# Optimization experiments

Hardware: AMD Instinct MI355X
Metric: run time of the kernel (lower is better)

Reference implementation:

```python
import jax, jax.numpy as jnp
import numpy as np

N_NODES = 10000
N_EDGES = 160000
NUM_FEAT = 14
EDGE_DIM = 4
DIM = 64        # hidden_channels
HID = 128       # GENConv MLP expansion = 2
LAYERS = 28
MSG_EPS = 1e-7  # GENConv eps added to relu(message)
LN_EPS = 1e-5   # torch LayerNorm default


def layernorm(h, g, b):
    mu = jnp.mean(h, axis=-1, keepdims=True)
    var = jnp.mean(jnp.square(h - mu), axis=-1, keepdims=True)
    return (h - mu) * jax.lax.rsqrt(var + LN_EPS) * g + b


def gen_conv(x, ea, src, dst, t, W1, b1, g1, be1, W2, b2):
    # message: relu(x_j + edge_attr) + eps  -> [E, D]
    msg = jax.nn.relu(x[src] + ea) + MSG_EPS
    # softmax aggregation over edges grouped by destination node
    logits = msg * t
    m = jax.ops.segment_max(logits, dst, num_segments=N_NODES)
    e = jnp.exp(logits - m[dst])
    s = jax.ops.segment_sum(e, dst, num_segments=N_NODES)
    alpha = e / (s[dst] + 1e-16)
    agg = jax.ops.segment_sum(msg * alpha, dst, num_segments=N_NODES)
    # residual + MLP [D -> 2D -> D] with LayerNorm+ReLU in between
    h = agg + x
    h = jax.nn.relu(layernorm(h @ W1 + b1, g1, be1))
    return h @ W2 + b2


def setup_inputs() -> dict:
    key = jax.random.key(0)
    ks = jax.random.split(key, 24)
    sc = 0.05
    inp = {
        "x": jax.random.normal(ks[0], (N_NODES, NUM_FEAT), jnp.float32),
        "edge_attr": jax.random.normal(ks[1], (N_EDGES, EDGE_DIM), jnp.float32),
        "src": jax.random.randint(ks[2], (N_EDGES,), 0, N_NODES, jnp.int32),
        "dst": jax.random.randint(ks[3], (N_EDGES,), 0, N_NODES, jnp.int32),
        # encoders
        "W_node": jax.random.normal(ks[4], (NUM_FEAT, DIM), jnp.float32) * sc,
        "b_node": jnp.zeros((DIM,), jnp.float32),
        "W_edge": jax.random.normal(ks[5], (EDGE_DIM, DIM), jnp.float32) * sc,
        "b_edge": jnp.zeros((DIM,), jnp.float32),
        # per-layer GENConv params (stacked over LAYERS)
        "t": jnp.ones((LAYERS,), jnp.float32),
        "W1": jax.random.normal(ks[6], (LAYERS, DIM, HID), jnp.float32) * sc,
        "b1": jnp.zeros((LAYERS, HID), jnp.float32),
        "g1": jnp.ones((LAYERS, HID), jnp.float32),
        "be1": jnp.zeros((LAYERS, HID), jnp.float32),
        "W2": jax.random.normal(ks[7], (LAYERS, HID, DIM), jnp.float32) * sc,
        "b2": jnp.zeros((LAYERS, DIM), jnp.float32),
        # per-layer DeepGCNLayer LayerNorm
        "ln_g": jnp.ones((LAYERS, DIM), jnp.float32),
        "ln_b": jnp.zeros((LAYERS, DIM), jnp.float32),
        # output projection
        "W_out": jax.random.normal(ks[8], (DIM, DIM), jnp.float32) * sc,
        "b_out": jnp.zeros((DIM,), jnp.float32),
    }
    return inp


def reference(x, edge_attr, src, dst, W_node, b_node, W_edge, b_edge,
              t, W1, b1, g1, be1, W2, b2, ln_g, ln_b, W_out, b_out):
    h = x @ W_node + b_node                  # node encoder  [N, D]
    ea = edge_attr @ W_edge + b_edge         # edge encoder  [E, D]

    # layer 0: conv only (no res+ wrapper), per DeeperGCN.forward
    h = gen_conv(h, ea, src, dst, t[0], W1[0], b1[0], g1[0], be1[0], W2[0], b2[0])

    # layers 1..L-1: res+ block: x + conv(dropout(relu(norm(x))))  (eval: dropout = id)
    def step(hc, p):
        ti, w1, bb1, gg1, bbe1, w2, bb2, lg, lb = p
        u = jax.nn.relu(layernorm(hc, lg, lb))
        u = gen_conv(u, ea, src, dst, ti, w1, bb1, gg1, bbe1, w2, bb2)
        return hc + u, None

    rest = (t[1:], W1[1:], b1[1:], g1[1:], be1[1:], W2[1:], b2[1:], ln_g[1:], ln_b[1:])
    h, _ = jax.lax.scan(step, h, rest)

    # final: act(layers[0].norm(x)), dropout (eval: id), lin
    h = jax.nn.relu(layernorm(h, ln_g[0], ln_b[0]))
    return h @ W_out + b_out
```

## Files before the change

### kernel.cpp

```cpp
#include <hip/hip_runtime.h>
#include <hip/hip_cooperative_groups.h>

namespace cg = cooperative_groups;

#define N_NODES 10000
#define N_EDGES 160000
#define NUM_FEAT 14
#define DIM 64
#define HID 128
#define LAYERS 28

#define NPB 20
#define NLB (N_NODES / NPB)
#define TPB 640

__device__ __forceinline__ void stage16(const float* gsrc, float* lds_base) {
  __builtin_amdgcn_global_load_lds(
      (const __attribute__((address_space(1))) void*)gsrc,
      (__attribute__((address_space(3))) void*)lds_base, 16, 0, 0);
}


__global__ __launch_bounds__(256) void k_hist(const int* __restrict__ dst, int* __restrict__ cur) {
  int e = blockIdx.x * 256 + threadIdx.x;
  if (e < N_EDGES) atomicAdd(&cur[dst[e]], 1);
}

__global__ __launch_bounds__(256) void k_scan(int* __restrict__ cur, int* __restrict__ off) {
  __shared__ int part[256];
  int t = threadIdx.x;
  const int CH = 40;
  int base = t * CH;
  int s = 0;
  for (int i = 0; i < CH; i++) {
    int idx = base + i;
    if (idx < N_NODES) s += cur[idx];
  }
  part[t] = s;
  __syncthreads();
  for (int ofs = 1; ofs < 256; ofs <<= 1) {
    int tmp = (t >= ofs) ? part[t - ofs] : 0;
    __syncthreads();
    part[t] += tmp;
    __syncthreads();
  }
  int run = part[t] - s;
  for (int i = 0; i < CH; i++) {
    int idx = base + i;
    if (idx < N_NODES) {
      int d = cur[idx];
      off[idx] = run;
      cur[idx] = run;
      run += d;
    }
  }
  if (t == 255) off[N_NODES] = part[255];
}

__global__ __launch_bounds__(256) void k_scatter(const int* __restrict__ dst, int* __restrict__ cur,
                                                 int* __restrict__ eids) {
  int e = blockIdx.x * 256 + threadIdx.x;
  if (e < N_EDGES) {
    int p = atomicAdd(&cur[dst[e]], 1);
    eids[p] = e;
  }
}

__global__ __launch_bounds__(256) void k_sortgather(
    const int* __restrict__ off, const int* __restrict__ eids,
    const int* __restrict__ src, const float4* __restrict__ eattr,
    const float* __restrict__ W_edge, const float* __restrict__ b_edge,
    int* __restrict__ src_s, float4* __restrict__ eattr_s, float* __restrict__ ea_s) {
  int node = blockIdx.x * 4 + (threadIdx.x >> 6);
  int lane = threadIdx.x & 63;
  if (node >= N_NODES) return;
  float we0 = W_edge[lane], we1 = W_edge[64 + lane], we2 = W_edge[128 + lane],
        we3 = W_edge[192 + lane];
  float be = b_edge[lane];
  int a = off[node];
  int d = off[node + 1] - a;
  if (d <= 64) {
    int key = (lane < d) ? eids[a + lane] : 0x7fffffff;
#pragma unroll
    for (int k = 2; k <= 64; k <<= 1) {
      for (int j = k >> 1; j > 0; j >>= 1) {
        int p = __shfl_xor(key, j);
        bool dirUp = ((lane & k) == 0);
        bool isLower = ((lane & j) == 0);
        key = ((isLower == dirUp) ? min(key, p) : max(key, p));
      }
    }
    float4 ev = make_float4(0.f, 0.f, 0.f, 0.f);
    if (lane < d) {
      src_s[a + lane] = src[key];
      ev = eattr[key];
    }
    for (int j = 0; j < d; j++) {
      float ex = __shfl(ev.x, j), ey = __shfl(ev.y, j),
            ez = __shfl(ev.z, j), ew = __shfl(ev.w, j);
      ea_s[(size_t)(a + j) * 64 + lane] =
          be + ex * we0 + ey * we1 + ez * we2 + ew * we3;
    }
  } else {
    for (int i = lane; i < d; i += 64) {
      int e = eids[a + i];
      int r = 0;
      for (int j = 0; j < d; j++) r += (eids[a + j] < e) ? 1 : 0;
      src_s[a + r] = src[e];
      eattr_s[a + r] = eattr[e];
    }
    for (int j = 0; j < d; j++) {
      float4 e4 = eattr_s[a + j];
      ea_s[(size_t)(a + j) * 64 + lane] =
          be + e4.x * we0 + e4.y * we1 + e4.z * we2 + e4.w * we3;
    }
  }
}


__global__ __launch_bounds__(256) void k_enc(const float* __restrict__ x, const float* __restrict__ Wn,
                                             const float* __restrict__ bn, float* __restrict__ hc,
                                             float* __restrict__ u) {
  int gid = blockIdx.x * 256 + threadIdx.x;
  if (gid >= N_NODES * DIM) return;
  int n = gid >> 6, j = gid & 63;
  float acc = bn[j];
#pragma unroll
  for (int k = 0; k < NUM_FEAT; k++) acc += x[n * NUM_FEAT + k] * Wn[k * DIM + j];
  hc[gid] = acc;
  u[gid] = acc;
}


__global__ __launch_bounds__(TPB, 5) void k_all(
    const float* __restrict__ x,
    const float* __restrict__ W_node, const float* __restrict__ b_node,
    const float* __restrict__ t,
    const float* __restrict__ W1a, const float* __restrict__ b1a,
    const float* __restrict__ g1a, const float* __restrict__ be1a,
    const float* __restrict__ W2a, const float* __restrict__ b2a,
    const float* __restrict__ ln_g, const float* __restrict__ ln_b,
    const float* __restrict__ W_out, const float* __restrict__ b_out,
    float* __restrict__ out,
    const float* __restrict__ ea_s, const int* __restrict__ src_s,
    const int* __restrict__ off,
    float* uA, float* uB) {
  cg::grid_group grid = cg::this_grid();

  __shared__ float sW1[64 * 128];
  __shared__ float sW2[128 * 64];
  __shared__ float sHZ[10][256];

  const int tid = threadIdx.x;
  const int lane = tid & 63;
  const int wv = tid >> 6;
  const int nbase = blockIdx.x * NPB;
  const int gn0 = __builtin_amdgcn_readfirstlane(nbase + wv * 2);
  const int gn1 = gn0 + 1;

  {
    float wn[NUM_FEAT];
#pragma unroll
    for (int f = 0; f < NUM_FEAT; f++) wn[f] = W_node[f * 64 + lane];
    float bn = b_node[lane];
    float a0 = bn, a1 = bn;
#pragma unroll
    for (int f = 0; f < NUM_FEAT; f++) {
      a0 = fmaf(x[gn0 * NUM_FEAT + f], wn[f], a0);
      a1 = fmaf(x[gn1 * NUM_FEAT + f], wn[f], a1);
    }
    uA[(gn0 << 6) + lane] = a0;
    uA[(gn1 << 6) + lane] = a1;
  }
  grid.sync();

  float hc0 = 0.f, hc1 = 0.f;

  for (int l = 0; l < LAYERS; l++) {
    const float* uin = (l & 1) ? uB : uA;
    float* uout = (l & 1) ? uA : uB;
    const float* W1 = W1a + (size_t)l * 64 * 128;
    const float* W2 = W2a + (size_t)l * 128 * 64;
    const float* b1 = b1a + (size_t)l * 128;
    const float* g1 = g1a + (size_t)l * 128;
    const float* be1 = be1a + (size_t)l * 128;
    const float* b2 = b2a + (size_t)l * 64;

    for (int c = wv; c < 32; c += 10) {
      stage16(W1 + c * 256 + lane * 4, sW1 + c * 256);
      stage16(W2 + c * 256 + lane * 4, sW2 + c * 256);
    }

    {
      float tv = t[l];
      float hpair[2];
#pragma unroll
      for (int q = 0; q < 2; q++) {
        int gn = (q == 0) ? gn0 : gn1;
        int a = off[gn], d = off[gn + 1] - a;
        float un = uin[(gn << 6) + lane];
        float s0 = 0.f, s1 = 0.f, ac0 = 0.f, ac1 = 0.f;
        int i = 0;
        for (; i + 8 <= d; i += 8) {
          float uv[8], ev[8];
#pragma unroll
          for (int j = 0; j < 8; j++) {
            int sn = src_s[a + i + j];
            uv[j] = uin[(sn << 6) + lane];
            ev[j] = ea_s[(size_t)(a + i + j) * 64 + lane];
          }
#pragma unroll
          for (int j = 0; j < 8; j++) {
            float msg = fmaxf(uv[j] + ev[j], 0.f) + 1e-7f;
            float e = __expf(msg * tv);
            if (j & 1) { s1 += e; ac1 = fmaf(e, msg, ac1); }
            else       { s0 += e; ac0 = fmaf(e, msg, ac0); }
          }
        }
        for (; i < d; i++) {
          int sn = src_s[a + i];
          float msg = fmaxf(uin[(sn << 6) + lane] + ea_s[(size_t)(a + i) * 64 + lane],
                            0.f) + 1e-7f;
          float e = __expf(msg * tv);
          s0 += e;
          ac0 = fmaf(e, msg, ac0);
        }
        hpair[q] = (ac0 + ac1) / (s0 + s1 + 1e-16f) + un;
      }
      *((float2*)&sHZ[wv][lane * 2]) = make_float2(hpair[0], hpair[1]);
    }
    __syncthreads();

    int j0 = 2 * lane;
    float2 b1v = *((const float2*)&b1[j0]);
    float a00 = b1v.x, a01 = b1v.y, a10 = b1v.x, a11 = b1v.y;
#pragma unroll 8
    for (int k = 0; k < 64; k++) {
      float2 hp = *((float2*)&sHZ[wv][k * 2]);
      float2 wp = *((float2*)&sW1[k * 128 + j0]);
      a00 += hp.x * wp.x; a01 += hp.x * wp.y;
      a10 += hp.y * wp.x; a11 += hp.y * wp.y;
    }

    {
      float2 gv = *((const float2*)&g1[j0]);
      float2 bev = *((const float2*)&be1[j0]);
      float s0 = a00 + a01, q0 = a00 * a00 + a01 * a01;
      float s1 = a10 + a11, q1 = a10 * a10 + a11 * a11;
#pragma unroll
      for (int o = 32; o; o >>= 1) {
        s0 += __shfl_xor(s0, o); q0 += __shfl_xor(q0, o);
        s1 += __shfl_xor(s1, o); q1 += __shfl_xor(q1, o);
      }
      float mu0 = s0 * (1.f / 128.f), mu1 = s1 * (1.f / 128.f);
      float rs0 = rsqrtf(q0 * (1.f / 128.f) - mu0 * mu0 + 1e-5f);
      float rs1 = rsqrtf(q1 * (1.f / 128.f) - mu1 * mu1 + 1e-5f);
      float4 zv;
      zv.x = fmaxf((a00 - mu0) * rs0 * gv.x + bev.x, 0.f);
      zv.y = fmaxf((a10 - mu1) * rs1 * gv.x + bev.x, 0.f);
      zv.z = fmaxf((a01 - mu0) * rs0 * gv.y + bev.y, 0.f);
      zv.w = fmaxf((a11 - mu1) * rs1 * gv.y + bev.y, 0.f);
      *((float4*)&sHZ[wv][4 * lane]) = zv;
    }

    float bo = b2[lane];
    float o0 = bo, o1 = bo;
#pragma unroll 8
    for (int k = 0; k < 128; k++) {
      float2 zp = *((float2*)&sHZ[wv][k * 2]);
      float wv2 = sW2[k * 64 + lane];
      o0 += zp.x * wv2;
      o1 += zp.y * wv2;
    }

    hc0 += o0;
    hc1 += o1;

    if (l < LAYERS - 1) {
      float lg_ = ln_g[(l + 1) * 64 + lane], lb_ = ln_b[(l + 1) * 64 + lane];
      float s0 = hc0, q0 = hc0 * hc0;
      float s1 = hc1, q1 = hc1 * hc1;
#pragma unroll
      for (int o = 32; o; o >>= 1) {
        s0 += __shfl_xor(s0, o); q0 += __shfl_xor(q0, o);
        s1 += __shfl_xor(s1, o); q1 += __shfl_xor(q1, o);
      }
      float mu0 = s0 * (1.f / 64.f), mu1 = s1 * (1.f / 64.f);
      float rs0 = rsqrtf(q0 * (1.f / 64.f) - mu0 * mu0 + 1e-5f);
      float rs1 = rsqrtf(q1 * (1.f / 64.f) - mu1 * mu1 + 1e-5f);
      uout[(gn0 << 6) + lane] = fmaxf((hc0 - mu0) * rs0 * lg_ + lb_, 0.f);
      uout[(gn1 << 6) + lane] = fmaxf((hc1 - mu1) * rs1 * lg_ + lb_, 0.f);
      grid.sync();
    }
  }

  __syncthreads();
  for (int c = wv; c < 16; c += 10) {
    stage16(W_out + c * 256 + lane * 4, sW1 + c * 256);
  }
  {
    float lg_ = ln_g[lane], lb_ = ln_b[lane];
    float s0 = hc0, q0 = hc0 * hc0;
    float s1 = hc1, q1 = hc1 * hc1;
#pragma unroll
    for (int o = 32; o; o >>= 1) {
      s0 += __shfl_xor(s0, o); q0 += __shfl_xor(q0, o);
      s1 += __shfl_xor(s1, o); q1 += __shfl_xor(q1, o);
    }
    float mu0 = s0 * (1.f / 64.f), mu1 = s1 * (1.f / 64.f);
    float rs0 = rsqrtf(q0 * (1.f / 64.f) - mu0 * mu0 + 1e-5f);
    float rs1 = rsqrtf(q1 * (1.f / 64.f) - mu1 * mu1 + 1e-5f);
    float z0 = fmaxf((hc0 - mu0) * rs0 * lg_ + lb_, 0.f);
    float z1 = fmaxf((hc1 - mu1) * rs1 * lg_ + lb_, 0.f);
    *((float2*)&sHZ[wv][lane * 2]) = make_float2(z0, z1);
  }
  __syncthreads();
  {
    float bo = b_out[lane];
    float o0 = bo, o1 = bo;
#pragma unroll 8
    for (int k = 0; k < 64; k++) {
      float2 zp = *((float2*)&sHZ[wv][k * 2]);
      float wv2 = sW1[k * 64 + lane];
      o0 += zp.x * wv2;
      o1 += zp.y * wv2;
    }
    out[(gn0 << 6) + lane] = o0;
    out[(gn1 << 6) + lane] = o1;
  }
}


__global__ __launch_bounds__(640, 5) void k_layer(
    const float* __restrict__ uin, float* __restrict__ hc, float* __restrict__ uout,
    const float* __restrict__ ea_s, const int* __restrict__ src_s,
    const int* __restrict__ off, const float* __restrict__ tptr, int layer,
    const float* __restrict__ W1, const float* __restrict__ b1,
    const float* __restrict__ g1, const float* __restrict__ be1,
    const float* __restrict__ W2, const float* __restrict__ b2,
    const float* __restrict__ lng, const float* __restrict__ lnb,
    int addRes, int writeU) {
  __shared__ float sW1[64 * 128];
  __shared__ float sW2[128 * 64];
  __shared__ float sHZ[10][256];

  const int tid = threadIdx.x;
  const int lane = tid & 63;
  const int wv = tid >> 6;
  const int nbase = blockIdx.x * NPB;

  for (int c = wv; c < 32; c += 10) {
    stage16(W1 + c * 256 + lane * 4, sW1 + c * 256);
    stage16(W2 + c * 256 + lane * 4, sW2 + c * 256);
  }

  {
    float tv = tptr[layer];
    float hpair[2];
#pragma unroll
    for (int q = 0; q < 2; q++) {
      int gn = __builtin_amdgcn_readfirstlane(nbase + wv * 2 + q);
      int a = off[gn], d = off[gn + 1] - a;
      float un = uin[(gn << 6) + lane];
      float s0 = 0.f, s1 = 0.f, ac0 = 0.f, ac1 = 0.f;
      int i = 0;
      for (; i + 8 <= d; i += 8) {
        float uv[8], ev[8];
#pragma unroll
        for (int j = 0; j < 8; j++) {
          int sn = src_s[a + i + j];
          uv[j] = uin[(sn << 6) + lane];
          ev[j] = ea_s[(size_t)(a + i + j) * 64 + lane];
        }
#pragma unroll
        for (int j = 0; j < 8; j++) {
          float msg = fmaxf(uv[j] + ev[j], 0.f) + 1e-7f;
          float e = __expf(msg * tv);
          if (j & 1) { s1 += e; ac1 = fmaf(e, msg, ac1); }
          else       { s0 += e; ac0 = fmaf(e, msg, ac0); }
        }
      }
      for (; i < d; i++) {
        int sn = src_s[a + i];
        float msg = fmaxf(uin[(sn << 6) + lane] + ea_s[(size_t)(a + i) * 64 + lane],
                          0.f) + 1e-7f;
        float e = __expf(msg * tv);
        s0 += e;
        ac0 = fmaf(e, msg, ac0);
      }
      hpair[q] = (ac0 + ac1) / (s0 + s1 + 1e-16f) + un;
    }
    *((float2*)&sHZ[wv][lane * 2]) = make_float2(hpair[0], hpair[1]);
  }
  __syncthreads();

  const int gn0 = nbase + wv * 2;
  const int gn1 = gn0 + 1;

  int j0 = 2 * lane;
  float2 b1v = *((const float2*)&b1[j0]);
  float a00 = b1v.x, a01 = b1v.y, a10 = b1v.x, a11 = b1v.y;
#pragma unroll 8
  for (int k = 0; k < 64; k++) {
    float2 hp = *((float2*)&sHZ[wv][k * 2]);
    float2 wp = *((float2*)&sW1[k * 128 + j0]);
    a00 += hp.x * wp.x; a01 += hp.x * wp.y;
    a10 += hp.y * wp.x; a11 += hp.y * wp.y;
  }

  {
    float2 gv = *((const float2*)&g1[j0]);
    float2 bev = *((const float2*)&be1[j0]);
    float s0 = a00 + a01, q0 = a00 * a00 + a01 * a01;
    float s1 = a10 + a11, q1 = a10 * a10 + a11 * a11;
#pragma unroll
    for (int o = 32; o; o >>= 1) {
      s0 += __shfl_xor(s0, o); q0 += __shfl_xor(q0, o);
      s1 += __shfl_xor(s1, o); q1 += __shfl_xor(q1, o);
    }
    float mu0 = s0 * (1.f / 128.f), mu1 = s1 * (1.f / 128.f);
    float rs0 = rsqrtf(q0 * (1.f / 128.f) - mu0 * mu0 + 1e-5f);
    float rs1 = rsqrtf(q1 * (1.f / 128.f) - mu1 * mu1 + 1e-5f);
    float4 zv;
    zv.x = fmaxf((a00 - mu0) * rs0 * gv.x + bev.x, 0.f);
    zv.y = fmaxf((a10 - mu1) * rs1 * gv.x + bev.x, 0.f);
    zv.z = fmaxf((a01 - mu0) * rs0 * gv.y + bev.y, 0.f);
    zv.w = fmaxf((a11 - mu1) * rs1 * gv.y + bev.y, 0.f);
    *((float4*)&sHZ[wv][4 * lane]) = zv;
  }

  float bo = b2[lane];
  float o0 = bo, o1 = bo;
#pragma unroll 8
  for (int k = 0; k < 128; k++) {
    float2 zp = *((float2*)&sHZ[wv][k * 2]);
    float wv2 = sW2[k * 64 + lane];
    o0 += zp.x * wv2;
    o1 += zp.y * wv2;
  }

  float r0 = addRes ? hc[gn0 * 64 + lane] : 0.f;
  float r1 = addRes ? hc[gn1 * 64 + lane] : 0.f;
  float hcn0 = o0 + r0, hcn1 = o1 + r1;
  hc[gn0 * 64 + lane] = hcn0;
  hc[gn1 * 64 + lane] = hcn1;

  if (writeU) {
    float lg_ = lng[lane], lb_ = lnb[lane];
    float s0 = hcn0, q0 = hcn0 * hcn0;
    float s1 = hcn1, q1 = hcn1 * hcn1;
#pragma unroll
    for (int o = 32; o; o >>= 1) {
      s0 += __shfl_xor(s0, o); q0 += __shfl_xor(q0, o);
      s1 += __shfl_xor(s1, o); q1 += __shfl_xor(q1, o);
    }
    float mu0 = s0 * (1.f / 64.f), mu1 = s1 * (1.f / 64.f);
    float rs0 = rsqrtf(q0 * (1.f / 64.f) - mu0 * mu0 + 1e-5f);
    float rs1 = rsqrtf(q1 * (1.f / 64.f) - mu1 * mu1 + 1e-5f);
    uout[gn0 * 64 + lane] = fmaxf((hcn0 - mu0) * rs0 * lg_ + lb_, 0.f);
    uout[gn1 * 64 + lane] = fmaxf((hcn1 - mu1) * rs1 * lg_ + lb_, 0.f);
  }
}

__global__ __launch_bounds__(256) void k_final(const float* __restrict__ hc, const float* __restrict__ g,
                                               const float* __restrict__ bptr, const float* __restrict__ Wout,
                                               const float* __restrict__ bout, float* __restrict__ out) {
  __shared__ float sW[DIM * DIM];
  int tid = threadIdx.x;
  for (int i = tid; i < 1024; i += 256) ((float4*)sW)[i] = ((const float4*)Wout)[i];
  __syncthreads();
  int lane = tid & 63, w = tid >> 6;
  int n = blockIdx.x * 4 + w;
  if (n >= N_NODES) return;
  float v = hc[n * 64 + lane];
  float s = v, q = v * v;
#pragma unroll
  for (int o = 32; o; o >>= 1) { s += __shfl_xor(s, o); q += __shfl_xor(q, o); }
  float mu = s * (1.f / 64.f);
  float var = q * (1.f / 64.f) - mu * mu;
  float rs = rsqrtf(var + 1e-5f);
  float z = fmaxf((v - mu) * rs * g[lane] + bptr[lane], 0.f);
  float acc = bout[lane];
  for (int k = 0; k < 64; k++) {
    float zk = __shfl(z, k);
    acc += zk * sW[k * 64 + lane];
  }
  out[n * 64 + lane] = acc;
}


extern "C" void kernel_launch(void* const* d_in, const int* in_sizes, int n_in,
                              void* d_out, int out_size, void* d_ws, size_t ws_size,
                              hipStream_t stream) {
  const float* x        = (const float*)d_in[0];
  const float* eattr    = (const float*)d_in[1];
  const int*   src      = (const int*)d_in[2];
  const int*   dst      = (const int*)d_in[3];
  const float* W_node   = (const float*)d_in[4];
  const float* b_node   = (const float*)d_in[5];
  const float* W_edge   = (const float*)d_in[6];
  const float* b_edge   = (const float*)d_in[7];
  const float* t        = (const float*)d_in[8];
  const float* W1       = (const float*)d_in[9];
  const float* b1       = (const float*)d_in[10];
  const float* g1       = (const float*)d_in[11];
  const float* be1      = (const float*)d_in[12];
  const float* W2       = (const float*)d_in[13];
  const float* b2       = (const float*)d_in[14];
  const float* ln_g     = (const float*)d_in[15];
  const float* ln_b     = (const float*)d_in[16];
  const float* W_out    = (const float*)d_in[17];
  const float* b_out    = (const float*)d_in[18];
  float* out = (float*)d_out;

  char* w = (char*)d_ws;
  float* uA      = (float*)w;  w += (size_t)N_NODES * 64 * 4;
  float* uB      = (float*)w;  w += (size_t)N_NODES * 64 * 4;
  float* hcb     = (float*)w;  w += (size_t)N_NODES * 64 * 4;
  int* off       = (int*)w;    w += (size_t)(N_NODES + 1) * 4;
  int* cur       = (int*)w;    w += (size_t)N_NODES * 4;
  int* eids      = (int*)w;    w += (size_t)N_EDGES * 4;
  int* src_s     = (int*)w;    w += (size_t)N_EDGES * 4;
  float4* eattr_s = (float4*)w; w += (size_t)N_EDGES * 16;
  float* ea_s    = (float*)w;  w += (size_t)N_EDGES * 64 * 4;

  hipMemsetAsync(cur, 0, (size_t)N_NODES * 4, stream);
  k_hist<<<(N_EDGES + 255) / 256, 256, 0, stream>>>(dst, cur);
  k_scan<<<1, 256, 0, stream>>>(cur, off);
  k_scatter<<<(N_EDGES + 255) / 256, 256, 0, stream>>>(dst, cur, eids);
  k_sortgather<<<(N_NODES + 3) / 4, 256, 0, stream>>>(off, eids, src, (const float4*)eattr,
                                                      W_edge, b_edge, src_s, eattr_s, ea_s);

  int maxBlocksPerCU = 0;
  hipError_t qerr = hipOccupancyMaxActiveBlocksPerMultiprocessor(&maxBlocksPerCU, k_all, TPB, 0);
  int dev = 0, nCU = 0;
  hipGetDevice(&dev);
  hipDeviceGetAttribute(&nCU, hipDeviceAttributeMultiprocessorCount, dev);
  bool coop_ok = (qerr == hipSuccess) && ((long)maxBlocksPerCU * (long)nCU >= (long)NLB);

  hipError_t lerr = hipErrorUnknown;
  if (coop_ok) {
    void* args[] = {
        (void*)&x, (void*)&W_node, (void*)&b_node, (void*)&t,
        (void*)&W1, (void*)&b1, (void*)&g1, (void*)&be1, (void*)&W2, (void*)&b2,
        (void*)&ln_g, (void*)&ln_b, (void*)&W_out, (void*)&b_out,
        (void*)&out, (void*)&ea_s, (void*)&src_s, (void*)&off,
        (void*)&uA, (void*)&uB};
    lerr = hipLaunchCooperativeKernel((const void*)k_all, dim3(NLB), dim3(TPB), args, 0, stream);
  }
  if (!coop_ok || lerr != hipSuccess) {
    k_enc<<<(N_NODES * 64 + 255) / 256, 256, 0, stream>>>(x, W_node, b_node, hcb, uA);
    for (int l = 0; l < LAYERS; l++) {
      const float* uin = (l & 1) ? uB : uA;
      float* uo        = (l & 1) ? uA : uB;
      int nxt = (l + 1 < LAYERS) ? (l + 1) : 0;
      k_layer<<<NLB, 640, 0, stream>>>(uin, hcb, uo, ea_s, src_s, off, t, l,
                                       W1 + (size_t)l * DIM * HID, b1 + (size_t)l * HID,
                                       g1 + (size_t)l * HID, be1 + (size_t)l * HID,
                                       W2 + (size_t)l * HID * DIM, b2 + (size_t)l * DIM,
                                       ln_g + (size_t)nxt * DIM, ln_b + (size_t)nxt * DIM,
                                       (l > 0) ? 1 : 0, (l < LAYERS - 1) ? 1 : 0);
    }
    k_final<<<(N_NODES + 3) / 4, 256, 0, stream>>>(hcb, ln_g, ln_b, W_out, b_out, out);
  }
}
```

Before: 925.3 us.

## Halve cooperative grid so each block handles two node tiles per layer

The persistent cooperative kernel now launches 250 blocks instead of 500, and each wave processes four nodes (two in each half of the node range) per layer. Each block stages the per-layer W1/W2 weights into LDS once and reuses them for twice as many nodes, and fewer blocks take part in each grid-wide barrier. The cost is half as many resident waves for hiding gather latency, more serial work per wave, and a larger shared buffer.

```diff
diff --git a/kernel.cpp b/kernel.cpp
--- a/kernel.cpp
+++ b/kernel.cpp
@@ -13,6 +13,8 @@
 #define NPB 20
 #define NLB (N_NODES / NPB)
 #define TPB 640
+#define CBLK 250
+#define TILEB 5000
 
 __device__ __forceinline__ void stage16(const float* gsrc, float* lds_base) {
   __builtin_amdgcn_global_load_lds(
@@ -132,6 +134,42 @@
 }
 
 
+__device__ __forceinline__ float edge_node(
+    int gn, const float* __restrict__ uin, const float* __restrict__ ea_s,
+    const int* __restrict__ src_s, const int* __restrict__ off,
+    int lane, float tv) {
+  int a = off[gn], d = off[gn + 1] - a;
+  float un = uin[(gn << 6) + lane];
+  float s0 = 0.f, s1 = 0.f, ac0 = 0.f, ac1 = 0.f;
+  int i = 0;
+  for (; i + 8 <= d; i += 8) {
+    float uv[8], ev[8];
+#pragma unroll
+    for (int j = 0; j < 8; j++) {
+      int sn = src_s[a + i + j];
+      uv[j] = uin[(sn << 6) + lane];
+      ev[j] = ea_s[(size_t)(a + i + j) * 64 + lane];
+    }
+#pragma unroll
+    for (int j = 0; j < 8; j++) {
+      float msg = fmaxf(uv[j] + ev[j], 0.f) + 1e-7f;
+      float e = __expf(msg * tv);
+      if (j & 1) { s1 += e; ac1 = fmaf(e, msg, ac1); }
+      else       { s0 += e; ac0 = fmaf(e, msg, ac0); }
+    }
+  }
+  for (; i < d; i++) {
+    int sn = src_s[a + i];
+    float msg = fmaxf(uin[(sn << 6) + lane] + ea_s[(size_t)(a + i) * 64 + lane],
+                      0.f) + 1e-7f;
+    float e = __expf(msg * tv);
+    s0 += e;
+    ac0 = fmaf(e, msg, ac0);
+  }
+  return (ac0 + ac1) / (s0 + s1 + 1e-16f) + un;
+}
+
+
 __global__ __launch_bounds__(TPB, 5) void k_all(
     const float* __restrict__ x,
     const float* __restrict__ W_node, const float* __restrict__ b_node,
@@ -149,32 +187,37 @@
 
   __shared__ float sW1[64 * 128];
   __shared__ float sW2[128 * 64];
-  __shared__ float sHZ[10][256];
+  __shared__ float sHZ[10][512];
 
   const int tid = threadIdx.x;
   const int lane = tid & 63;
   const int wv = tid >> 6;
-  const int nbase = blockIdx.x * NPB;
-  const int gn0 = __builtin_amdgcn_readfirstlane(nbase + wv * 2);
-  const int gn1 = gn0 + 1;
+  const int gnA0 = __builtin_amdgcn_readfirstlane(blockIdx.x * NPB + wv * 2);
+  const int gnA1 = gnA0 + 1;
+  const int gnB0 = gnA0 + TILEB;
+  const int gnB1 = gnB0 + 1;
 
   {
     float wn[NUM_FEAT];
 #pragma unroll
     for (int f = 0; f < NUM_FEAT; f++) wn[f] = W_node[f * 64 + lane];
     float bn = b_node[lane];
-    float a0 = bn, a1 = bn;
+    float a0 = bn, a1 = bn, b0 = bn, b1v = bn;
 #pragma unroll
     for (int f = 0; f < NUM_FEAT; f++) {
-      a0 = fmaf(x[gn0 * NUM_FEAT + f], wn[f], a0);
-      a1 = fmaf(x[gn1 * NUM_FEAT + f], wn[f], a1);
-    }
-    uA[(gn0 << 6) + lane] = a0;
-    uA[(gn1 << 6) + lane] = a1;
+      a0 = fmaf(x[gnA0 * NUM_FEAT + f], wn[f], a0);
+      a1 = fmaf(x[gnA1 * NUM_FEAT + f], wn[f], a1);
+      b0 = fmaf(x[gnB0 * NUM_FEAT + f], wn[f], b0);
+      b1v = fmaf(x[gnB1 * NUM_FEAT + f], wn[f], b1v);
+    }
+    uA[(gnA0 << 6) + lane] = a0;
+    uA[(gnA1 << 6) + lane] = a1;
+    uA[(gnB0 << 6) + lane] = b0;
+    uA[(gnB1 << 6) + lane] = b1v;
   }
   grid.sync();
 
-  float hc0 = 0.f, hc1 = 0.f;
+  float hcA0 = 0.f, hcA1 = 0.f, hcB0 = 0.f, hcB1 = 0.f;
 
   for (int l = 0; l < LAYERS; l++) {
     const float* uin = (l & 1) ? uB : uA;
@@ -193,105 +236,87 @@
 
     {
       float tv = t[l];
-      float hpair[2];
-#pragma unroll
-      for (int q = 0; q < 2; q++) {
-        int gn = (q == 0) ? gn0 : gn1;
-        int a = off[gn], d = off[gn + 1] - a;
-        float un = uin[(gn << 6) + lane];
-        float s0 = 0.f, s1 = 0.f, ac0 = 0.f, ac1 = 0.f;
-        int i = 0;
-        for (; i + 8 <= d; i += 8) {
-          float uv[8], ev[8];
-#pragma unroll
-          for (int j = 0; j < 8; j++) {
-            int sn = src_s[a + i + j];
-            uv[j] = uin[(sn << 6) + lane];
-            ev[j] = ea_s[(size_t)(a + i + j) * 64 + lane];
-          }
-#pragma unroll
-          for (int j = 0; j < 8; j++) {
-            float msg = fmaxf(uv[j] + ev[j], 0.f) + 1e-7f;
-            float e = __expf(msg * tv);
-            if (j & 1) { s1 += e; ac1 = fmaf(e, msg, ac1); }
-            else       { s0 += e; ac0 = fmaf(e, msg, ac0); }
-          }
+      float hA0 = edge_node(gnA0, uin, ea_s, src_s, off, lane, tv);
+      float hA1 = edge_node(gnA1, uin, ea_s, src_s, off, lane, tv);
+      *((float2*)&sHZ[wv][lane * 2]) = make_float2(hA0, hA1);
+      float hB0 = edge_node(gnB0, uin, ea_s, src_s, off, lane, tv);
+      float hB1 = edge_node(gnB1, uin, ea_s, src_s, off, lane, tv);
+      *((float2*)&sHZ[wv][128 + lane * 2]) = make_float2(hB0, hB1);
+    }
+    __syncthreads();
+
+#pragma unroll
+    for (int tb = 0; tb < 2; tb++) {
+      const int hbase = tb * 128;
+      float* hcp0 = tb ? &hcB0 : &hcA0;
+      float* hcp1 = tb ? &hcB1 : &hcA1;
+      const int g0 = tb ? gnB0 : gnA0;
+      const int g1i = tb ? gnB1 : gnA1;
+
+      int j0 = 2 * lane;
+      float2 b1p = *((const float2*)&b1[j0]);
+      float a00 = b1p.x, a01 = b1p.y, a10 = b1p.x, a11 = b1p.y;
+#pragma unroll 8
+      for (int k = 0; k < 64; k++) {
+        float2 hp = *((float2*)&sHZ[wv][hbase + k * 2]);
+        float2 wp = *((float2*)&sW1[k * 128 + j0]);
+        a00 += hp.x * wp.x; a01 += hp.x * wp.y;
+        a10 += hp.y * wp.x; a11 += hp.y * wp.y;
+      }
+
+      {
+        float2 gv = *((const float2*)&g1[j0]);
+        float2 bev = *((const float2*)&be1[j0]);
+        float s0 = a00 + a01, q0 = a00 * a00 + a01 * a01;
+        float s1 = a10 + a11, q1 = a10 * a10 + a11 * a11;
+#pragma unroll
+        for (int o = 32; o; o >>= 1) {
+          s0 += __shfl_xor(s0, o); q0 += __shfl_xor(q0, o);
+          s1 += __shfl_xor(s1, o); q1 += __shfl_xor(q1, o);
         }
-        for (; i < d; i++) {
-          int sn = src_s[a + i];
-          float msg = fmaxf(uin[(sn << 6) + lane] + ea_s[(size_t)(a + i) * 64 + lane],
-                            0.f) + 1e-7f;
-          float e = __expf(msg * tv);
-          s0 += e;
-          ac0 = fmaf(e, msg, ac0);
+        float mu0 = s0 * (1.f / 128.f), mu1 = s1 * (1.f / 128.f);
+        float rs0 = rsqrtf(q0 * (1.f / 128.f) - mu0 * mu0 + 1e-5f);
+        float rs1 = rsqrtf(q1 * (1.f / 128.f) - mu1 * mu1 + 1e-5f);
+        float4 zv;
+        zv.x = fmaxf((a00 - mu0) * rs0 * gv.x + bev.x, 0.f);
+        zv.y = fmaxf((a10 - mu1) * rs1 * gv.x + bev.x, 0.f);
+        zv.z = fmaxf((a01 - mu0) * rs0 * gv.y + bev.y, 0.f);
+        zv.w = fmaxf((a11 - mu1) * rs1 * gv.y + bev.y, 0.f);
+        *((float4*)&sHZ[wv][256 + 4 * lane]) = zv;
+      }
+
+      float bo = b2[lane];
+      float o0 = bo, o1 = bo;
+#pragma unroll 8
+      for (int k = 0; k < 128; k++) {
+        float2 zp = *((float2*)&sHZ[wv][256 + k * 2]);
+        float wv2 = sW2[k * 64 + lane];
+        o0 += zp.x * wv2;
+        o1 += zp.y * wv2;
+      }
+
+      *hcp0 += o0;
+      *hcp1 += o1;
+
+      if (l < LAYERS - 1) {
+        float lg_ = ln_g[(l + 1) * 64 + lane], lb_ = ln_b[(l + 1) * 64 + lane];
+        float h0 = *hcp0, h1 = *hcp1;
+        float s0 = h0, q0 = h0 * h0;
+        float s1 = h1, q1 = h1 * h1;
+#pragma unroll
+        for (int o = 32; o; o >>= 1) {
+          s0 += __shfl_xor(s0, o); q0 += __shfl_xor(q0, o);
+          s1 += __shfl_xor(s1, o); q1 += __shfl_xor(q1, o);
         }
-        hpair[q] = (ac0 + ac1) / (s0 + s1 + 1e-16f) + un;
+        float mu0 = s0 * (1.f / 64.f), mu1 = s1 * (1.f / 64.f);
+        float rs0 = rsqrtf(q0 * (1.f / 64.f) - mu0 * mu0 + 1e-5f);
+        float rs1 = rsqrtf(q1 * (1.f / 64.f) - mu1 * mu1 + 1e-5f);
+        uout[(g0 << 6) + lane] = fmaxf((h0 - mu0) * rs0 * lg_ + lb_, 0.f);
+        uout[(g1i << 6) + lane] = fmaxf((h1 - mu1) * rs1 * lg_ + lb_, 0.f);
       }
-      *((float2*)&sHZ[wv][lane * 2]) = make_float2(hpair[0], hpair[1]);
-    }
-    __syncthreads();
-
-    int j0 = 2 * lane;
-    float2 b1v = *((const float2*)&b1[j0]);
-    float a00 = b1v.x, a01 = b1v.y, a10 = b1v.x, a11 = b1v.y;
-#pragma unroll 8
-    for (int k = 0; k < 64; k++) {
-      float2 hp = *((float2*)&sHZ[wv][k * 2]);
-      float2 wp = *((float2*)&sW1[k * 128 + j0]);
-      a00 += hp.x * wp.x; a01 += hp.x * wp.y;
-      a10 += hp.y * wp.x; a11 += hp.y * wp.y;
-    }
-
-    {
-      float2 gv = *((const float2*)&g1[j0]);
-      float2 bev = *((const float2*)&be1[j0]);
-      float s0 = a00 + a01, q0 = a00 * a00 + a01 * a01;
-      float s1 = a10 + a11, q1 = a10 * a10 + a11 * a11;
-#pragma unroll
-      for (int o = 32; o; o >>= 1) {
-        s0 += __shfl_xor(s0, o); q0 += __shfl_xor(q0, o);
-        s1 += __shfl_xor(s1, o); q1 += __shfl_xor(q1, o);
-      }
-      float mu0 = s0 * (1.f / 128.f), mu1 = s1 * (1.f / 128.f);
-      float rs0 = rsqrtf(q0 * (1.f / 128.f) - mu0 * mu0 + 1e-5f);
-      float rs1 = rsqrtf(q1 * (1.f / 128.f) - mu1 * mu1 + 1e-5f);
-      float4 zv;
-      zv.x = fmaxf((a00 - mu0) * rs0 * gv.x + bev.x, 0.f);
-      zv.y = fmaxf((a10 - mu1) * rs1 * gv.x + bev.x, 0.f);
-      zv.z = fmaxf((a01 - mu0) * rs0 * gv.y + bev.y, 0.f);
-      zv.w = fmaxf((a11 - mu1) * rs1 * gv.y + bev.y, 0.f);
-      *((float4*)&sHZ[wv][4 * lane]) = zv;
-    }
-
-    float bo = b2[lane];
-    float o0 = bo, o1 = bo;
-#pragma unroll 8
-    for (int k = 0; k < 128; k++) {
-      float2 zp = *((float2*)&sHZ[wv][k * 2]);
-      float wv2 = sW2[k * 64 + lane];
-      o0 += zp.x * wv2;
-      o1 += zp.y * wv2;
-    }
-
-    hc0 += o0;
-    hc1 += o1;
-
-    if (l < LAYERS - 1) {
-      float lg_ = ln_g[(l + 1) * 64 + lane], lb_ = ln_b[(l + 1) * 64 + lane];
-      float s0 = hc0, q0 = hc0 * hc0;
-      float s1 = hc1, q1 = hc1 * hc1;
-#pragma unroll
-      for (int o = 32; o; o >>= 1) {
-        s0 += __shfl_xor(s0, o); q0 += __shfl_xor(q0, o);
-        s1 += __shfl_xor(s1, o); q1 += __shfl_xor(q1, o);
-      }
-      float mu0 = s0 * (1.f / 64.f), mu1 = s1 * (1.f / 64.f);
-      float rs0 = rsqrtf(q0 * (1.f / 64.f) - mu0 * mu0 + 1e-5f);
-      float rs1 = rsqrtf(q1 * (1.f / 64.f) - mu1 * mu1 + 1e-5f);
-      uout[(gn0 << 6) + lane] = fmaxf((hc0 - mu0) * rs0 * lg_ + lb_, 0.f);
-      uout[(gn1 << 6) + lane] = fmaxf((hc1 - mu1) * rs1 * lg_ + lb_, 0.f);
-      grid.sync();
-    }
+    }
+
+    if (l < LAYERS - 1) grid.sync();
   }
 
   __syncthreads();
@@ -300,33 +325,36 @@
   }
   {
     float lg_ = ln_g[lane], lb_ = ln_b[lane];
-    float s0 = hc0, q0 = hc0 * hc0;
-    float s1 = hc1, q1 = hc1 * hc1;
-#pragma unroll
-    for (int o = 32; o; o >>= 1) {
-      s0 += __shfl_xor(s0, o); q0 += __shfl_xor(q0, o);
-      s1 += __shfl_xor(s1, o); q1 += __shfl_xor(q1, o);
-    }
-    float mu0 = s0 * (1.f / 64.f), mu1 = s1 * (1.f / 64.f);
-    float rs0 = rsqrtf(q0 * (1.f / 64.f) - mu0 * mu0 + 1e-5f);
-    float rs1 = rsqrtf(q1 * (1.f / 64.f) - mu1 * mu1 + 1e-5f);
-    float z0 = fmaxf((hc0 - mu0) * rs0 * lg_ + lb_, 0.f);
-    float z1 = fmaxf((hc1 - mu1) * rs1 * lg_ + lb_, 0.f);
-    *((float2*)&sHZ[wv][lane * 2]) = make_float2(z0, z1);
+    float v[4] = {hcA0, hcA1, hcB0, hcB1};
+#pragma unroll
+    for (int q = 0; q < 4; q++) {
+      float s = v[q], qq = v[q] * v[q];
+#pragma unroll
+      for (int o = 32; o; o >>= 1) { s += __shfl_xor(s, o); qq += __shfl_xor(qq, o); }
+      float mu = s * (1.f / 64.f);
+      float rs = rsqrtf(qq * (1.f / 64.f) - mu * mu + 1e-5f);
+      float z = fmaxf((v[q] - mu) * rs * lg_ + lb_, 0.f);
+      sHZ[wv][(q >> 1) * 128 + (q & 1) + lane * 2] = z;
+    }
   }
   __syncthreads();
   {
     float bo = b_out[lane];
-    float o0 = bo, o1 = bo;
+    float oA0 = bo, oA1 = bo, oB0 = bo, oB1 = bo;
 #pragma unroll 8
     for (int k = 0; k < 64; k++) {
-      float2 zp = *((float2*)&sHZ[wv][k * 2]);
+      float2 zpA = *((float2*)&sHZ[wv][k * 2]);
+      float2 zpB = *((float2*)&sHZ[wv][128 + k * 2]);
       float wv2 = sW1[k * 64 + lane];
-      o0 += zp.x * wv2;
-      o1 += zp.y * wv2;
-    }
-    out[(gn0 << 6) + lane] = o0;
-    out[(gn1 << 6) + lane] = o1;
+      oA0 += zpA.x * wv2;
+      oA1 += zpA.y * wv2;
+      oB0 += zpB.x * wv2;
+      oB1 += zpB.y * wv2;
+    }
+    out[(gnA0 << 6) + lane] = oA0;
+    out[(gnA1 << 6) + lane] = oA1;
+    out[(gnB0 << 6) + lane] = oB0;
+    out[(gnB1 << 6) + lane] = oB1;
   }
 }
 
@@ -360,35 +388,7 @@
 #pragma unroll
     for (int q = 0; q < 2; q++) {
       int gn = __builtin_amdgcn_readfirstlane(nbase + wv * 2 + q);
-      int a = off[gn], d = off[gn + 1] - a;
-      float un = uin[(gn << 6) + lane];
-      float s0 = 0.f, s1 = 0.f, ac0 = 0.f, ac1 = 0.f;
-      int i = 0;
-      for (; i + 8 <= d; i += 8) {
-        float uv[8], ev[8];
-#pragma unroll
-        for (int j = 0; j < 8; j++) {
-          int sn = src_s[a + i + j];
-          uv[j] = uin[(sn << 6) + lane];
-          ev[j] = ea_s[(size_t)(a + i + j) * 64 + lane];
-        }
-#pragma unroll
-        for (int j = 0; j < 8; j++) {
-          float msg = fmaxf(uv[j] + ev[j], 0.f) + 1e-7f;
-          float e = __expf(msg * tv);
-          if (j & 1) { s1 += e; ac1 = fmaf(e, msg, ac1); }
-          else       { s0 += e; ac0 = fmaf(e, msg, ac0); }
-        }
-      }
-      for (; i < d; i++) {
-        int sn = src_s[a + i];
-        float msg = fmaxf(uin[(sn << 6) + lane] + ea_s[(size_t)(a + i) * 64 + lane],
-                          0.f) + 1e-7f;
-        float e = __expf(msg * tv);
-        s0 += e;
-        ac0 = fmaf(e, msg, ac0);
-      }
-      hpair[q] = (ac0 + ac1) / (s0 + s1 + 1e-16f) + un;
+      hpair[q] = edge_node(gn, uin, ea_s, src_s, off, lane, tv);
     }
     *((float2*)&sHZ[wv][lane * 2]) = make_float2(hpair[0], hpair[1]);
   }
@@ -536,7 +536,7 @@
   int dev = 0, nCU = 0;
   hipGetDevice(&dev);
   hipDeviceGetAttribute(&nCU, hipDeviceAttributeMultiprocessorCount, dev);
-  bool coop_ok = (qerr == hipSuccess) && ((long)maxBlocksPerCU * (long)nCU >= (long)NLB);
+  bool coop_ok = (qerr == hipSuccess) && ((long)maxBlocksPerCU * (long)nCU >= (long)CBLK);
 
   hipError_t lerr = hipErrorUnknown;
   if (coop_ok) {
@@ -546,7 +546,7 @@
         (void*)&ln_g, (void*)&ln_b, (void*)&W_out, (void*)&b_out,
         (void*)&out, (void*)&ea_s, (void*)&src_s, (void*)&off,
         (void*)&uA, (void*)&uB};
-    lerr = hipLaunchCooperativeKernel((const void*)k_all, dim3(NLB), dim3(TPB), args, 0, stream);
+    lerr = hipLaunchCooperativeKernel((const void*)k_all, dim3(CBLK), dim3(TPB), args, 0, stream);
   }
   if (!coop_ok || lerr != hipSuccess) {
     k_enc<<<(N_NODES * 64 + 255) / 256, 256, 0, stream>>>(x, W_node, b_node, hcb, uA);
```

Measured after the change: 927.0 us. About the same (+0.2%).
